# Optimization experiments

Measured on AMD Instinct MI355X. Metric: run time of the kernel, lower is better.

Reference implementation:

```python
import jax, jax.numpy as jnp
import numpy as np

B, T, H, FUT = 256, 512, 128, 512


def setup_inputs() -> dict:
    key = jax.random.key(0)
    ks = jax.random.split(key, 24)
    s = 1.0 / np.sqrt(H)

    def u(k, shape, scale):
        return jax.random.uniform(k, shape, jnp.float32, -scale, scale)

    inp = {
        "input": jax.random.normal(ks[0], (B, T), jnp.float32),
        "future": FUT,
        # LSTMCell 1 (input size 1)
        "Wih1": u(ks[1], (4 * H, 1), s), "Whh1": u(ks[2], (4 * H, H), s),
        "bih1": u(ks[3], (4 * H,), s), "bhh1": u(ks[4], (4 * H,), s),
        # LSTMCell 2
        "Wih2": u(ks[5], (4 * H, H), s), "Whh2": u(ks[6], (4 * H, H), s),
        "bih2": u(ks[7], (4 * H,), s), "bhh2": u(ks[8], (4 * H,), s),
        # LSTMCell 3
        "Wih3": u(ks[9], (4 * H, H), s), "Whh3": u(ks[10], (4 * H, H), s),
        "bih3": u(ks[11], (4 * H,), s), "bhh3": u(ks[12], (4 * H,), s),
        # MultiheadAttention packed in-proj (q,k,v) and out-proj
        "in_proj_w": u(ks[13], (3 * H, H), s), "in_proj_b": u(ks[14], (3 * H,), s),
        "out_w": u(ks[15], (H, H), s), "out_b": u(ks[16], (H,), s),
        # final Linear(H, 1)
        "lin_w": u(ks[17], (1, H), s), "lin_b": u(ks[18], (1,), s),
    }
    return inp


def _lstm_cell(x, h, c, Wih, Whh, bih, bhh):
    # torch LSTMCell gate order: i, f, g, o
    g = x @ Wih.T + h @ Whh.T + (bih + bhh)
    i, f, gg, o = jnp.split(g, 4, axis=-1)
    c_new = jax.nn.sigmoid(f) * c + jax.nn.sigmoid(i) * jnp.tanh(gg)
    h_new = jax.nn.sigmoid(o) * jnp.tanh(c_new)
    return h_new, c_new


def _forward(input, Wih1, Whh1, bih1, bhh1, Wih2, Whh2, bih2, bhh2,
             Wih3, Whh3, bih3, bhh3, in_proj_w, in_proj_b, out_w, out_b,
             lin_w, lin_b, future):
    hd = in_proj_w.shape[1]
    # seq_len == 1 attention: softmax over a single key is 1, so
    # attn_output = out_proj(v_proj(h3)); q/k play no role in the output.
    Wv = in_proj_w[2 * hd:]
    bv = in_proj_b[2 * hd:]

    def head(h3):
        attn = (h3 @ Wv.T + bv) @ out_w.T + out_b
        return attn @ lin_w.T + lin_b  # [B, 1]

    def step(states, x_t):
        h1, c1, h2, c2, h3, c3 = states
        h1, c1 = _lstm_cell(x_t, h1, c1, Wih1, Whh1, bih1, bhh1)
        h2, c2 = _lstm_cell(h1, h2, c2, Wih2, Whh2, bih2, bhh2)
        h3, c3 = _lstm_cell(h2, h3, c3, Wih3, Whh3, bih3, bhh3)
        return (h1, c1, h2, c2, h3, c3), head(h3)

    n = input.shape[0]
    z = jnp.zeros((n, hd), input.dtype)
    init = (z, z, z, z, z, z)

    xs = input.T[:, :, None]  # [T, B, 1]
    states, outs = jax.lax.scan(lambda s, x: step(s, x), init, xs)

    def fstep(carry, _):
        st, out = carry
        st, out = step(st, out)
        return (st, out), out

    (_, _), fouts = jax.lax.scan(fstep, (states, outs[-1]), None, length=future)
    all_outs = jnp.concatenate([outs, fouts], axis=0)  # [T+future, B, 1]
    return all_outs[..., 0].T  # [B, T+future]


def reference(input, Wih1, Whh1, bih1, bhh1, Wih2, Whh2, bih2, bhh2,
              Wih3, Whh3, bih3, bhh3, in_proj_w, in_proj_b, out_w, out_b,
              lin_w, lin_b, future):
    return _forward(input, Wih1, Whh1, bih1, bhh1, Wih2, Whh2, bih2, bhh2,
                    Wih3, Whh3, bih3, bhh3, in_proj_w, in_proj_b, out_w,
                    out_b, lin_w, lin_b, future)
```

## Files before the change

### kernel.cpp

```cpp
#include <hip/hip_runtime.h>


typedef _Float16 f16;
typedef _Float16 f16x2 __attribute__((ext_vector_type(2)));
typedef unsigned int u32;

#define T_IN 512
#define T_TOT 1024
#define NBLK 128

__device__ __forceinline__ f16x2 u2h(u32 u) { return __builtin_bit_cast(f16x2, u); }

__device__ __forceinline__ float fdot2f(f16x2 a, f16x2 b, float c) {
#if __has_builtin(__builtin_amdgcn_fdot2)
  return __builtin_amdgcn_fdot2(a, b, c, false);
#else
  return c + (float)a[0] * (float)b[0] + (float)a[1] * (float)b[1];
#endif
}

__device__ __forceinline__ float frcp(float x) {
#if __has_builtin(__builtin_amdgcn_rcpf)
  return __builtin_amdgcn_rcpf(x);
#else
  return 1.f / x;
#endif
}
__device__ __forceinline__ float fsigm(float x) { return frcp(1.f + __expf(-x)); }
__device__ __forceinline__ float ftanh(float x) { return 1.f - 2.f * frcp(1.f + __expf(2.f * x)); }

#define DOT4(acc, w, hv)                     \
  do {                                       \
    f16x2 _h = u2h(hv);                      \
    acc[0] = fdot2f(u2h((w).x), _h, acc[0]); \
    acc[1] = fdot2f(u2h((w).y), _h, acc[1]); \
    acc[2] = fdot2f(u2h((w).z), _h, acc[2]); \
    acc[3] = fdot2f(u2h((w).w), _h, acc[3]); \
  } while (0)

__global__ void pack_stream(u32* dst, const float* Wih2, const float* Whh2,
                            const float* Wih3, const float* Whh3) {
  int tid = blockIdx.x * 256 + threadIdx.x;
  if (tid >= 64 * 512 * 4) return;
  int g = tid & 3;
  int t = (tid >> 2) & 511;
  int s = tid >> 11;
  int idx = t >> 2, kq = t & 3;
  const float* src;
  int p;
  if (s < 48) {
    int q = s / 6, rmd = s % 6;
    if (rmd < 4) {
      p = kq * 32 + 4 * q + rmd;
      if (p < 64) { src = Wih2; } else { src = Whh2; p -= 64; }
    } else {
      p = kq * 16 + 2 * q + (rmd - 4);
      src = Whh3;
    }
  } else {
    p = kq * 16 + (s - 48);
    src = Wih3;
  }
  int j = g * 128 + idx;
  union { f16 h[2]; u32 u; } cv;
  cv.h[0] = (f16)src[j * 128 + 2 * p];
  cv.h[1] = (f16)src[j * 128 + 2 * p + 1];
  dst[tid] = cv.u;
}

__global__ void pack1s(u32* dst, const float* Whh1) {
  int tid = blockIdx.x * 256 + threadIdx.x;
  if (tid >= 16 * 512 * 4) return;
  int g = tid & 3;
  int t = (tid >> 2) & 511;
  int q = tid >> 11;
  int idx = t >> 2, kq = t & 3;
  int p = kq * 16 + q;
  int j = g * 128 + idx;
  union { f16 h[2]; u32 u; } cv;
  cv.h[0] = (f16)Whh1[j * 128 + 2 * p];
  cv.h[1] = (f16)Whh1[j * 128 + 2 * p + 1];
  dst[tid] = cv.u;
}

__global__ void prep_cons(float* cons, const float* a1, const float* b1,
                          const float* a2, const float* b2,
                          const float* a3, const float* b3, const float* wih1) {
  int tid = blockIdx.x * 256 + threadIdx.x;
  if (tid >= 2048) return;
  int gg = tid >> 9, g = (tid >> 7) & 3, idx = tid & 127;
  int j = g * 128 + idx;
  float v;
  if (gg == 0) v = a1[j] + b1[j];
  else if (gg == 1) v = a2[j] + b2[j];
  else if (gg == 2) v = a3[j] + b3[j];
  else v = wih1[j];
  cons[tid] = v;
}

__global__ void head_fold(float* cons, const float* lin_w, const float* out_w,
                          const float* Wv, const float* bv,
                          const float* out_b, const float* lin_b) {
  __shared__ float wlo[128];
  __shared__ float pr[128];
  int j = threadIdx.x;
  float s = 0.f;
  for (int k = 0; k < 128; ++k) s += lin_w[k] * out_w[k * 128 + j];
  wlo[j] = s;
  __syncthreads();
  float t = 0.f;
  for (int k = 0; k < 128; ++k) t += wlo[k] * Wv[k * 128 + j];
  cons[2048 + j] = t;
  pr[j] = s * bv[j] + lin_w[j] * out_b[j];
  __syncthreads();
  if (j == 0) {
    float b = lin_b[0];
    for (int k = 0; k < 128; ++k) b += pr[k];
    cons[2176] = b;
  }
}

__global__ __launch_bounds__(512)
__attribute__((amdgpu_waves_per_eu(2))) void pendulum_persist(
    const float* __restrict__ input, const uint4* __restrict__ WT1s,
    const uint4* __restrict__ WS, const float* __restrict__ consG,
    float* __restrict__ out) {
  __shared__ __align__(16) uint4 w1s[8192];
  __shared__ __align__(16) f16 h1b[2][2][128];
  __shared__ __align__(16) f16 h2b[2][2][128];
  __shared__ __align__(16) f16 h3b[2][128];
  __shared__ float consL[2180];
  __shared__ float redp[2][8];

  const int t = threadIdx.x;
  const int idx = t >> 2;
  const int kq = t & 3;
  const int row0 = blockIdx.x * 2, row1 = row0 + 1;

  for (int e = t; e < 8192; e += 512) w1s[e] = WT1s[e];
  for (int e = t; e < 2177; e += 512) consL[e] = consG[e];
  if (t < 128) {
    h1b[0][0][t] = (f16)0.f; h1b[0][1][t] = (f16)0.f;
    h1b[1][0][t] = (f16)0.f; h1b[1][1][t] = (f16)0.f;
    h2b[0][0][t] = (f16)0.f; h2b[0][1][t] = (f16)0.f;
    h2b[1][0][t] = (f16)0.f; h2b[1][1][t] = (f16)0.f;
    h3b[0][t] = (f16)0.f;    h3b[1][t] = (f16)0.f;
  }

  const uint4* Wp = WS + t;
  const uint4* w1p = w1s + t;

  float c1a = 0.f, c1b = 0.f, c2a = 0.f, c2b = 0.f, c3a = 0.f, c3b = 0.f;
  float y0 = 0.f, y1 = 0.f;
  __syncthreads();
  const float beffv = consL[2176];

  {
    float x0 = input[row0 * T_IN], x1 = input[row1 * T_IN];
    if (kq == 0) {
      float b0 = consL[idx], b2v = consL[256 + idx], b3v = consL[384 + idx];
      float w0 = consL[1536 + idx], w2w = consL[1792 + idx],
            w3w = consL[1920 + idx];
      {
        float ig = fsigm(b0 + x0 * w0);
        float gg = ftanh(b2v + x0 * w2w), og = fsigm(b3v + x0 * w3w);
        c1a = ig * gg; h1b[0][0][idx] = (f16)(og * ftanh(c1a));
      }
      {
        float ig = fsigm(b0 + x1 * w0);
        float gg = ftanh(b2v + x1 * w2w), og = fsigm(b3v + x1 * w3w);
        c1b = ig * gg; h1b[0][1][idx] = (f16)(og * ftanh(c1b));
      }
    }
    __syncthreads();
  }

  uint4 ring[8];
#pragma unroll
  for (int c = 0; c < 8; ++c) ring[c] = Wp[c * 512];

  for (int s = 0; s < T_TOT; ++s) {
    const int par = s & 1;
    const int xi = (s + 1 < T_IN) ? (s + 1) : 0;
    float xl0 = input[row0 * T_IN + xi];
    float xl1 = input[row1 * T_IN + xi];

    const uint4* hL2r0 = (kq < 2)
        ? (const uint4*)&h1b[par][0][0] + kq * 8
        : (const uint4*)&h2b[par ^ 1][0][0] + (kq - 2) * 8;
    const uint4* hL2r1 = (kq < 2)
        ? (const uint4*)&h1b[par][1][0] + kq * 8
        : (const uint4*)&h2b[par ^ 1][1][0] + (kq - 2) * 8;
    const uint4* h3r0 = (const uint4*)&h3b[0][0] + kq * 4;
    const uint4* h3r1 = (const uint4*)&h3b[1][0] + kq * 4;

    float a2r0[4] = {0, 0, 0, 0}, a2r1[4] = {0, 0, 0, 0};
    float a3r0[4] = {0, 0, 0, 0}, a3r1[4] = {0, 0, 0, 0};

    uint4 E0, E1;
#pragma unroll
    for (int q = 0; q < 8; ++q) {
      uint4 H0 = hL2r0[q], H1 = hL2r1[q];
      u32 e0[4] = {H0.x, H0.y, H0.z, H0.w};
      u32 e1[4] = {H1.x, H1.y, H1.z, H1.w};
      if ((q & 1) == 0) { E0 = h3r0[q >> 1]; E1 = h3r1[q >> 1]; }
#pragma unroll
      for (int m = 0; m < 4; ++m) {
        const int sl = 6 * q + m;
        uint4 w = ring[sl & 7];
        ring[sl & 7] = Wp[((sl + 8) & 63) * 512];
        DOT4(a2r0, w, e0[m]);
        DOT4(a2r1, w, e1[m]);
      }
      {
        const int sl = 6 * q + 4;
        uint4 w = ring[sl & 7];
        ring[sl & 7] = Wp[((sl + 8) & 63) * 512];
        u32 h0 = (q & 1) ? E0.z : E0.x, h1v = (q & 1) ? E1.z : E1.x;
        DOT4(a3r0, w, h0);
        DOT4(a3r1, w, h1v);
      }
      {
        const int sl = 6 * q + 5;
        uint4 w = ring[sl & 7];
        ring[sl & 7] = Wp[((sl + 8) & 63) * 512];
        u32 h0 = (q & 1) ? E0.w : E0.y, h1v = (q & 1) ? E1.w : E1.y;
        DOT4(a3r0, w, h0);
        DOT4(a3r1, w, h1v);
      }
    }

#pragma unroll
    for (int g = 0; g < 4; ++g) {
      a2r0[g] += __shfl_xor(a2r0[g], 1, 64); a2r0[g] += __shfl_xor(a2r0[g], 2, 64);
      a2r1[g] += __shfl_xor(a2r1[g], 1, 64); a2r1[g] += __shfl_xor(a2r1[g], 2, 64);
    }
    if (kq == 0) {
      float b0 = consL[512 + idx], b1v = consL[640 + idx],
            b2v = consL[768 + idx], b3v = consL[896 + idx];
      {
        float ig = fsigm(a2r0[0] + b0), fg = fsigm(a2r0[1] + b1v);
        float gg = ftanh(a2r0[2] + b2v), og = fsigm(a2r0[3] + b3v);
        c2a = fg * c2a + ig * gg;
        h2b[par][0][idx] = (f16)(og * ftanh(c2a));
      }
      {
        float ig = fsigm(a2r1[0] + b0), fg = fsigm(a2r1[1] + b1v);
        float gg = ftanh(a2r1[2] + b2v), og = fsigm(a2r1[3] + b3v);
        c2b = fg * c2b + ig * gg;
        h2b[par][1][idx] = (f16)(og * ftanh(c2b));
      }
    }
    asm volatile("s_waitcnt lgkmcnt(0)\n\ts_barrier" ::: "memory");

    const uint4* hLTr0 = (const uint4*)&h2b[par][0][0] + kq * 4;
    const uint4* hLTr1 = (const uint4*)&h2b[par][1][0] + kq * 4;
    const uint4* h1r0 = (const uint4*)&h1b[par][0][0] + kq * 4;
    const uint4* h1r1 = (const uint4*)&h1b[par][1][0] + kq * 4;

    float a1r0[4] = {0, 0, 0, 0}, a1r1[4] = {0, 0, 0, 0};
    uint4 L0, L1v, F0, F1;
#pragma unroll
    for (int q = 0; q < 8; ++q) {
      if ((q & 1) == 0) {
        L0 = hLTr0[q >> 1]; L1v = hLTr1[q >> 1];
        F0 = h1r0[q >> 1];  F1 = h1r1[q >> 1];
      }
      {
        const int sl = 48 + 2 * q;
        uint4 w = ring[sl & 7];
        ring[sl & 7] = Wp[((sl + 8) & 63) * 512];
        u32 h0 = (q & 1) ? L0.z : L0.x, h1x = (q & 1) ? L1v.z : L1v.x;
        DOT4(a3r0, w, h0);
        DOT4(a3r1, w, h1x);
      }
      {
        const int sl = 48 + 2 * q + 1;
        uint4 w = ring[sl & 7];
        ring[sl & 7] = Wp[((sl + 8) & 63) * 512];
        u32 h0 = (q & 1) ? L0.w : L0.y, h1x = (q & 1) ? L1v.w : L1v.y;
        DOT4(a3r0, w, h0);
        DOT4(a3r1, w, h1x);
      }
      {
        uint4 w = w1p[(2 * q) * 512];
        u32 h0 = (q & 1) ? F0.z : F0.x, h1x = (q & 1) ? F1.z : F1.x;
        DOT4(a1r0, w, h0);
        DOT4(a1r1, w, h1x);
      }
      {
        uint4 w = w1p[(2 * q + 1) * 512];
        u32 h0 = (q & 1) ? F0.w : F0.y, h1x = (q & 1) ? F1.w : F1.y;
        DOT4(a1r0, w, h0);
        DOT4(a1r1, w, h1x);
      }
    }

#pragma unroll
    for (int g = 0; g < 4; ++g) {
      a3r0[g] += __shfl_xor(a3r0[g], 1, 64); a3r0[g] += __shfl_xor(a3r0[g], 2, 64);
      a3r1[g] += __shfl_xor(a3r1[g], 1, 64); a3r1[g] += __shfl_xor(a3r1[g], 2, 64);
      a1r0[g] += __shfl_xor(a1r0[g], 1, 64); a1r0[g] += __shfl_xor(a1r0[g], 2, 64);
      a1r1[g] += __shfl_xor(a1r1[g], 1, 64); a1r1[g] += __shfl_xor(a1r1[g], 2, 64);
    }

    float p0 = 0.f, p1 = 0.f;
    if (kq == 0) {
      float b0 = consL[1024 + idx], b1v = consL[1152 + idx],
            b2v = consL[1280 + idx], b3v = consL[1408 + idx];
      float weffr = consL[2048 + idx];
      {
        float ig = fsigm(a3r0[0] + b0), fg = fsigm(a3r0[1] + b1v);
        float gg = ftanh(a3r0[2] + b2v), og = fsigm(a3r0[3] + b3v);
        c3a = fg * c3a + ig * gg;
        float h3 = og * ftanh(c3a);
        h3b[0][idx] = (f16)h3;
        p0 = weffr * h3;
      }
      {
        float ig = fsigm(a3r1[0] + b0), fg = fsigm(a3r1[1] + b1v);
        float gg = ftanh(a3r1[2] + b2v), og = fsigm(a3r1[3] + b3v);
        c3b = fg * c3b + ig * gg;
        float h3 = og * ftanh(c3b);
        h3b[1][idx] = (f16)h3;
        p1 = weffr * h3;
      }
    }
#pragma unroll
    for (int k = 1; k < 64; k <<= 1) {
      p0 += __shfl_xor(p0, k, 64);
      p1 += __shfl_xor(p1, k, 64);
    }
    if ((t & 63) == 0) { redp[0][t >> 6] = p0; redp[1][t >> 6] = p1; }
    asm volatile("s_waitcnt lgkmcnt(0)\n\ts_barrier" ::: "memory");

    y0 = beffv; y1 = beffv;
#pragma unroll
    for (int w8 = 0; w8 < 8; ++w8) { y0 += redp[0][w8]; y1 += redp[1][w8]; }
    if (t == 0) out[row0 * T_TOT + s] = y0;
    else if (t == 1) out[row1 * T_TOT + s] = y1;

    float xv0 = (s + 1 < T_IN) ? xl0 : y0;
    float xv1 = (s + 1 < T_IN) ? xl1 : y1;
    if (kq == 0) {
      float b0 = consL[idx], b1v = consL[128 + idx], b2v = consL[256 + idx],
            b3v = consL[384 + idx];
      float w0 = consL[1536 + idx], w1w = consL[1664 + idx],
            w2w = consL[1792 + idx], w3w = consL[1920 + idx];
      {
        float ig = fsigm(a1r0[0] + b0 + xv0 * w0), fg = fsigm(a1r0[1] + b1v + xv0 * w1w);
        float gg = ftanh(a1r0[2] + b2v + xv0 * w2w), og = fsigm(a1r0[3] + b3v + xv0 * w3w);
        c1a = fg * c1a + ig * gg;
        h1b[par ^ 1][0][idx] = (f16)(og * ftanh(c1a));
      }
      {
        float ig = fsigm(a1r1[0] + b0 + xv1 * w0), fg = fsigm(a1r1[1] + b1v + xv1 * w1w);
        float gg = ftanh(a1r1[2] + b2v + xv1 * w2w), og = fsigm(a1r1[3] + b3v + xv1 * w3w);
        c1b = fg * c1b + ig * gg;
        h1b[par ^ 1][1][idx] = (f16)(og * ftanh(c1b));
      }
    }
    asm volatile("s_waitcnt lgkmcnt(0)\n\ts_barrier" ::: "memory");
  }
}

extern "C" void kernel_launch(void* const* d_in, const int* in_sizes, int n_in,
                              void* d_out, int out_size, void* d_ws, size_t ws_size,
                              hipStream_t stream) {
  const float* input = (const float*)d_in[0];
  const float* Wih1 = (const float*)d_in[2];
  const float* Whh1 = (const float*)d_in[3];
  const float* bih1 = (const float*)d_in[4];
  const float* bhh1 = (const float*)d_in[5];
  const float* Wih2 = (const float*)d_in[6];
  const float* Whh2 = (const float*)d_in[7];
  const float* bih2 = (const float*)d_in[8];
  const float* bhh2 = (const float*)d_in[9];
  const float* Wih3 = (const float*)d_in[10];
  const float* Whh3 = (const float*)d_in[11];
  const float* bih3 = (const float*)d_in[12];
  const float* bhh3 = (const float*)d_in[13];
  const float* in_proj_w = (const float*)d_in[14];
  const float* in_proj_b = (const float*)d_in[15];
  const float* out_w = (const float*)d_in[16];
  const float* out_b = (const float*)d_in[17];
  const float* lin_w = (const float*)d_in[18];
  const float* lin_b = (const float*)d_in[19];

  char* ws = (char*)d_ws;
  u32* WT1s = (u32*)(ws + (0 << 10));
  u32* WS = (u32*)(ws + (128 << 10));
  float* consG = (float*)(ws + (640 << 10));

  pack1s<<<128, 256, 0, stream>>>(WT1s, Whh1);
  pack_stream<<<512, 256, 0, stream>>>(WS, Wih2, Whh2, Wih3, Whh3);
  prep_cons<<<8, 256, 0, stream>>>(consG, bih1, bhh1, bih2, bhh2, bih3, bhh3, Wih1);
  head_fold<<<1, 128, 0, stream>>>(consG, lin_w, out_w,
                                   in_proj_w + 2 * 128 * 128, in_proj_b + 256,
                                   out_b, lin_b);

  pendulum_persist<<<NBLK, 512, 0, stream>>>(
      input, (const uint4*)WT1s, (const uint4*)WS, consG, (float*)d_out);
}
```

Before: 9.069 ms.

## Stream all LSTM weights via global_load_lds ring buffer instead of register ring

Result: slower. 12.64 ms (+39.4%).

```diff
diff --git a/kernel.cpp b/kernel.cpp
--- a/kernel.cpp
+++ b/kernel.cpp
@@ -29,19 +29,24 @@
 __device__ __forceinline__ float fsigm(float x) { return frcp(1.f + __expf(-x)); }
 __device__ __forceinline__ float ftanh(float x) { return 1.f - 2.f * frcp(1.f + __expf(2.f * x)); }
 
-#define DOT4(acc, w, hv)                     \
-  do {                                       \
-    f16x2 _h = u2h(hv);                      \
-    acc[0] = fdot2f(u2h((w).x), _h, acc[0]); \
-    acc[1] = fdot2f(u2h((w).y), _h, acc[1]); \
-    acc[2] = fdot2f(u2h((w).z), _h, acc[2]); \
-    acc[3] = fdot2f(u2h((w).w), _h, acc[3]); \
-  } while (0)
+__device__ __forceinline__ void dot4(float (&acc)[4], uint4 wv, u32 hv) {
+  f16x2 hh = u2h(hv);
+  acc[0] = fdot2f(u2h(wv.x), hh, acc[0]);
+  acc[1] = fdot2f(u2h(wv.y), hh, acc[1]);
+  acc[2] = fdot2f(u2h(wv.z), hh, acc[2]);
+  acc[3] = fdot2f(u2h(wv.w), hh, acc[3]);
+}
+
+__device__ __forceinline__ void gl_lds16(const void* g, void* l) {
+  __builtin_amdgcn_global_load_lds((const __attribute__((address_space(1))) u32*)g,
+                                   (__attribute__((address_space(3))) u32*)l, 16, 0, 0);
+}
 
 __global__ void pack_stream(u32* dst, const float* Wih2, const float* Whh2,
-                            const float* Wih3, const float* Whh3) {
+                            const float* Wih3, const float* Whh3,
+                            const float* Whh1) {
   int tid = blockIdx.x * 256 + threadIdx.x;
-  if (tid >= 64 * 512 * 4) return;
+  if (tid >= 80 * 512 * 4) return;
   int g = tid & 3;
   int t = (tid >> 2) & 511;
   int s = tid >> 11;
@@ -58,28 +63,14 @@
       src = Whh3;
     }
   } else {
-    p = kq * 16 + (s - 48);
-    src = Wih3;
-  }
-  int j = g * 128 + idx;
+    int j = (s - 48) >> 2, r = (s - 48) & 3;
+    if (r < 2) { p = kq * 16 + 2 * j + r; src = Wih3; }
+    else       { p = kq * 16 + 2 * j + (r - 2); src = Whh1; }
+  }
+  int jj = g * 128 + idx;
   union { f16 h[2]; u32 u; } cv;
-  cv.h[0] = (f16)src[j * 128 + 2 * p];
-  cv.h[1] = (f16)src[j * 128 + 2 * p + 1];
-  dst[tid] = cv.u;
-}
-
-__global__ void pack1s(u32* dst, const float* Whh1) {
-  int tid = blockIdx.x * 256 + threadIdx.x;
-  if (tid >= 16 * 512 * 4) return;
-  int g = tid & 3;
-  int t = (tid >> 2) & 511;
-  int q = tid >> 11;
-  int idx = t >> 2, kq = t & 3;
-  int p = kq * 16 + q;
-  int j = g * 128 + idx;
-  union { f16 h[2]; u32 u; } cv;
-  cv.h[0] = (f16)Whh1[j * 128 + 2 * p];
-  cv.h[1] = (f16)Whh1[j * 128 + 2 * p + 1];
+  cv.h[0] = (f16)src[jj * 128 + 2 * p];
+  cv.h[1] = (f16)src[jj * 128 + 2 * p + 1];
   dst[tid] = cv.u;
 }
 
@@ -120,25 +111,35 @@
   }
 }
 
-__global__ __launch_bounds__(512)
-__attribute__((amdgpu_waves_per_eu(2))) void pendulum_persist(
-    const float* __restrict__ input, const uint4* __restrict__ WT1s,
-    const uint4* __restrict__ WS, const float* __restrict__ consG,
-    float* __restrict__ out) {
-  __shared__ __align__(16) uint4 w1s[8192];
+#define CONSUME(sl, A0, A1, hv0, hv1)                                       \
+  do {                                                                      \
+    dot4(A0, wbuf[(sl) & 3], hv0);                                          \
+    dot4(A1, wbuf[(sl) & 3], hv1);                                          \
+    gl_lds16(WSt + (((sl) + 16) % 80) * 512, (void*)&ringL[(sl) & 15][wb]); \
+    asm volatile("s_waitcnt vmcnt(12)" ::: "memory");                       \
+    wbuf[(sl) & 3] = ringL[((sl) + 4) & 15][t];                             \
+  } while (0)
+
+__global__ __launch_bounds__(512) void pendulum_persist(
+    const float* __restrict__ input, const uint4* __restrict__ WS,
+    const float* __restrict__ consG, float* __restrict__ out) {
+  __shared__ __align__(16) uint4 ringL[16][512];
   __shared__ __align__(16) f16 h1b[2][2][128];
   __shared__ __align__(16) f16 h2b[2][2][128];
   __shared__ __align__(16) f16 h3b[2][128];
+  __shared__ float xin[2][T_IN];
   __shared__ float consL[2180];
   __shared__ float redp[2][8];
 
   const int t = threadIdx.x;
   const int idx = t >> 2;
   const int kq = t & 3;
+  const int wb = t & 448;
   const int row0 = blockIdx.x * 2, row1 = row0 + 1;
 
-  for (int e = t; e < 8192; e += 512) w1s[e] = WT1s[e];
   for (int e = t; e < 2177; e += 512) consL[e] = consG[e];
+  for (int e = t; e < 1024; e += 512)
+    xin[e >> 9][e & 511] = input[(row0 + (e >> 9)) * T_IN + (e & 511)];
   if (t < 128) {
     h1b[0][0][t] = (f16)0.f; h1b[0][1][t] = (f16)0.f;
     h1b[1][0][t] = (f16)0.f; h1b[1][1][t] = (f16)0.f;
@@ -147,8 +148,7 @@
     h3b[0][t] = (f16)0.f;    h3b[1][t] = (f16)0.f;
   }
 
-  const uint4* Wp = WS + t;
-  const uint4* w1p = w1s + t;
+  const uint4* WSt = WS + t;
 
   float c1a = 0.f, c1b = 0.f, c2a = 0.f, c2b = 0.f, c3a = 0.f, c3b = 0.f;
   float y0 = 0.f, y1 = 0.f;
@@ -156,7 +156,7 @@
   const float beffv = consL[2176];
 
   {
-    float x0 = input[row0 * T_IN], x1 = input[row1 * T_IN];
+    float x0 = xin[0][0], x1 = xin[1][0];
     if (kq == 0) {
       float b0 = consL[idx], b2v = consL[256 + idx], b3v = consL[384 + idx];
       float w0 = consL[1536 + idx], w2w = consL[1792 + idx],
@@ -175,15 +175,18 @@
     __syncthreads();
   }
 
-  uint4 ring[8];
-#pragma unroll
-  for (int c = 0; c < 8; ++c) ring[c] = Wp[c * 512];
+#pragma unroll
+  for (int c = 0; c < 16; ++c) gl_lds16(WSt + c * 512, (void*)&ringL[c][wb]);
+  asm volatile("s_waitcnt vmcnt(12)" ::: "memory");
+  uint4 wbuf[4];
+#pragma unroll
+  for (int c = 0; c < 4; ++c) wbuf[c] = ringL[c][t];
 
   for (int s = 0; s < T_TOT; ++s) {
     const int par = s & 1;
     const int xi = (s + 1 < T_IN) ? (s + 1) : 0;
-    float xl0 = input[row0 * T_IN + xi];
-    float xl1 = input[row1 * T_IN + xi];
+    float xl0 = xin[0][xi];
+    float xl1 = xin[1][xi];
 
     const uint4* hL2r0 = (kq < 2)
         ? (const uint4*)&h1b[par][0][0] + kq * 8
@@ -204,30 +207,14 @@
       u32 e0[4] = {H0.x, H0.y, H0.z, H0.w};
       u32 e1[4] = {H1.x, H1.y, H1.z, H1.w};
       if ((q & 1) == 0) { E0 = h3r0[q >> 1]; E1 = h3r1[q >> 1]; }
-#pragma unroll
-      for (int m = 0; m < 4; ++m) {
-        const int sl = 6 * q + m;
-        uint4 w = ring[sl & 7];
-        ring[sl & 7] = Wp[((sl + 8) & 63) * 512];
-        DOT4(a2r0, w, e0[m]);
-        DOT4(a2r1, w, e1[m]);
-      }
-      {
-        const int sl = 6 * q + 4;
-        uint4 w = ring[sl & 7];
-        ring[sl & 7] = Wp[((sl + 8) & 63) * 512];
-        u32 h0 = (q & 1) ? E0.z : E0.x, h1v = (q & 1) ? E1.z : E1.x;
-        DOT4(a3r0, w, h0);
-        DOT4(a3r1, w, h1v);
-      }
-      {
-        const int sl = 6 * q + 5;
-        uint4 w = ring[sl & 7];
-        ring[sl & 7] = Wp[((sl + 8) & 63) * 512];
-        u32 h0 = (q & 1) ? E0.w : E0.y, h1v = (q & 1) ? E1.w : E1.y;
-        DOT4(a3r0, w, h0);
-        DOT4(a3r1, w, h1v);
-      }
+      CONSUME(6 * q + 0, a2r0, a2r1, e0[0], e1[0]);
+      CONSUME(6 * q + 1, a2r0, a2r1, e0[1], e1[1]);
+      CONSUME(6 * q + 2, a2r0, a2r1, e0[2], e1[2]);
+      CONSUME(6 * q + 3, a2r0, a2r1, e0[3], e1[3]);
+      u32 ea0 = (q & 1) ? E0.z : E0.x, ea1 = (q & 1) ? E1.z : E1.x;
+      u32 eb0 = (q & 1) ? E0.w : E0.y, eb1 = (q & 1) ? E1.w : E1.y;
+      CONSUME(6 * q + 4, a3r0, a3r1, ea0, ea1);
+      CONSUME(6 * q + 5, a3r0, a3r1, eb0, eb1);
     }
 
 #pragma unroll
@@ -261,39 +248,19 @@
     float a1r0[4] = {0, 0, 0, 0}, a1r1[4] = {0, 0, 0, 0};
     uint4 L0, L1v, F0, F1;
 #pragma unroll
-    for (int q = 0; q < 8; ++q) {
-      if ((q & 1) == 0) {
-        L0 = hLTr0[q >> 1]; L1v = hLTr1[q >> 1];
-        F0 = h1r0[q >> 1];  F1 = h1r1[q >> 1];
-      }
-      {
-        const int sl = 48 + 2 * q;
-        uint4 w = ring[sl & 7];
-        ring[sl & 7] = Wp[((sl + 8) & 63) * 512];
-        u32 h0 = (q & 1) ? L0.z : L0.x, h1x = (q & 1) ? L1v.z : L1v.x;
-        DOT4(a3r0, w, h0);
-        DOT4(a3r1, w, h1x);
-      }
-      {
-        const int sl = 48 + 2 * q + 1;
-        uint4 w = ring[sl & 7];
-        ring[sl & 7] = Wp[((sl + 8) & 63) * 512];
-        u32 h0 = (q & 1) ? L0.w : L0.y, h1x = (q & 1) ? L1v.w : L1v.y;
-        DOT4(a3r0, w, h0);
-        DOT4(a3r1, w, h1x);
-      }
-      {
-        uint4 w = w1p[(2 * q) * 512];
-        u32 h0 = (q & 1) ? F0.z : F0.x, h1x = (q & 1) ? F1.z : F1.x;
-        DOT4(a1r0, w, h0);
-        DOT4(a1r1, w, h1x);
-      }
-      {
-        uint4 w = w1p[(2 * q + 1) * 512];
-        u32 h0 = (q & 1) ? F0.w : F0.y, h1x = (q & 1) ? F1.w : F1.y;
-        DOT4(a1r0, w, h0);
-        DOT4(a1r1, w, h1x);
-      }
+    for (int j = 0; j < 8; ++j) {
+      if ((j & 1) == 0) {
+        L0 = hLTr0[j >> 1]; L1v = hLTr1[j >> 1];
+        F0 = h1r0[j >> 1];  F1 = h1r1[j >> 1];
+      }
+      u32 la0 = (j & 1) ? L0.z : L0.x, la1 = (j & 1) ? L1v.z : L1v.x;
+      u32 lb0 = (j & 1) ? L0.w : L0.y, lb1 = (j & 1) ? L1v.w : L1v.y;
+      u32 fa0 = (j & 1) ? F0.z : F0.x, fa1 = (j & 1) ? F1.z : F1.x;
+      u32 fb0 = (j & 1) ? F0.w : F0.y, fb1 = (j & 1) ? F1.w : F1.y;
+      CONSUME(48 + 4 * j + 0, a3r0, a3r1, la0, la1);
+      CONSUME(48 + 4 * j + 1, a3r0, a3r1, lb0, lb1);
+      CONSUME(48 + 4 * j + 2, a1r0, a1r1, fa0, fa1);
+      CONSUME(48 + 4 * j + 3, a1r0, a1r1, fb0, fb1);
     }
 
 #pragma unroll
@@ -388,17 +355,15 @@
   const float* lin_b = (const float*)d_in[19];
 
   char* ws = (char*)d_ws;
-  u32* WT1s = (u32*)(ws + (0 << 10));
-  u32* WS = (u32*)(ws + (128 << 10));
+  u32* WS = (u32*)(ws + (0 << 10));
   float* consG = (float*)(ws + (640 << 10));
 
-  pack1s<<<128, 256, 0, stream>>>(WT1s, Whh1);
-  pack_stream<<<512, 256, 0, stream>>>(WS, Wih2, Whh2, Wih3, Whh3);
+  pack_stream<<<640, 256, 0, stream>>>(WS, Wih2, Whh2, Wih3, Whh3, Whh1);
   prep_cons<<<8, 256, 0, stream>>>(consG, bih1, bhh1, bih2, bhh2, bih3, bhh3, Wih1);
   head_fold<<<1, 128, 0, stream>>>(consG, lin_w, out_w,
                                    in_proj_w + 2 * 128 * 128, in_proj_b + 256,
                                    out_b, lin_b);
 
   pendulum_persist<<<NBLK, 512, 0, stream>>>(
-      input, (const uint4*)WT1s, (const uint4*)WS, consG, (float*)d_out);
-}
+      input, (const uint4*)WS, consG, (float*)d_out);
+}
```
